# Kernel optimization log

Hardware: AMD Instinct MI355X
Metric: run time of the kernel (lower is better)

## Reference

```python
import jax, jax.numpy as jnp
import numpy as np

N = 8192          # num nodes
F_DIM = 32        # input feature dim
E_DIM = 32        # embedding_dim
SUPPORT = 4       # num relations
NUM_BASES = 2     # basis decomposition size


def setup_inputs() -> dict:
    key = jax.random.key(0)
    k1, k2, k3, k4 = jax.random.split(key, 4)
    features = jax.random.normal(k1, (N, F_DIM), dtype=jnp.float32)
    A = jax.random.normal(k2, (SUPPORT, N, N), dtype=jnp.float32)
    W = jax.random.normal(k3, (NUM_BASES, F_DIM, E_DIM), dtype=jnp.float32) * 0.05
    W_comp = jax.random.normal(k4, (SUPPORT, NUM_BASES), dtype=jnp.float32) * 0.05
    return {"features": features, "A": A, "W": W, "W_comp": W_comp}


def reference(features, A, W, W_comp):
    # Per-relation aggregation: supports[s] = A[s] @ features  -> [S, N, F]
    supports = jnp.einsum('snm,mf->snf', A, features)
    # Concatenate along axis=1 (feature axis): column order is s-major (s*F + f)
    n = features.shape[0]
    supports_ = jnp.transpose(supports, (1, 0, 2)).reshape(n, SUPPORT * F_DIM)
    # Basis decomposition, exactly as original:
    # W: (B, F, E) -> transpose (F, B, E); V = W_comp @ W -> (F, S, E)
    Wt = jnp.transpose(W, (1, 0, 2))                       # [F, B, E]
    V = jnp.einsum('sb,fbe->fse', W_comp, Wt)              # [F, S, E]
    V = V.reshape(SUPPORT * F_DIM, E_DIM)                  # row order f-major (f*S + s), faithful to original
    return supports_ @ V                                   # [N, E]
```

## Files before the change

kernel.cpp:

```cpp
#include <hip/hip_runtime.h>

#define NND 8192
#define FD  32
#define ED  32
#define SUP 4
#define NB  2

#define BROWS 256
#define TK    32
#define CHUNK 2048
#define NSTEP (CHUNK/TK)

#define FMA4(acc, sa, g) { acc.x += (sa) * (g).x; acc.y += (sa) * (g).y; \
                           acc.z += (sa) * (g).z; acc.w += (sa) * (g).w; }

#define GLDS16(gsrc, ldst) \
  __builtin_amdgcn_global_load_lds((const __attribute__((address_space(1))) void*)(gsrc), \
                                   (__attribute__((address_space(3))) void*)(ldst), 16, 0, 0)

__global__ __launch_bounds__(256) void prep_g(
        const float* __restrict__ features,
        const float* __restrict__ W,
        const float* __restrict__ Wc,
        float* __restrict__ G,
        float* __restrict__ out) {
    __shared__ __align__(16) float Vlds[FD * ED];
    const int t   = threadIdx.x;
    const int gid = blockIdx.x * 256 + t;
    const int s   = gid >> 13;
    const int m   = gid & (NND - 1);

    for (int i = t; i < FD * ED; i += 256) {
        const int e  = i & 31;
        const int f  = i >> 5;
        const int f2 = s * 8 + (f >> 2);
        const int s2 = f & 3;
        float v = 0.f;
        #pragma unroll
        for (int b = 0; b < NB; ++b)
            v += Wc[s2 * NB + b] * W[(b * FD + f2) * ED + e];
        Vlds[i] = v;
    }
    __syncthreads();

    float4* out4 = (float4*)out;
    const float4 z = {0.f, 0.f, 0.f, 0.f};
    out4[gid]         = z;
    out4[gid + 32768] = z;

    const float4* feat4 = (const float4*)(features + (size_t)m * FD);
    float4 fr[8];
    #pragma unroll
    for (int i = 0; i < 8; ++i) fr[i] = feat4[i];

    float4 acc[8];
    #pragma unroll
    for (int i = 0; i < 8; ++i) acc[i] = z;

    const float4* V4 = (const float4*)Vlds;
    #pragma unroll
    for (int f = 0; f < FD; ++f) {
        const float fv = ((const float*)fr)[f];
        #pragma unroll
        for (int e4 = 0; e4 < 8; ++e4) {
            const float4 v = V4[f * 8 + e4];
            FMA4(acc[e4], fv, v);
        }
    }
    float4* g4 = (float4*)(G + ((size_t)s * NND + m) * ED);
    #pragma unroll
    for (int e4 = 0; e4 < 8; ++e4) g4[e4] = acc[e4];
}

__global__ __launch_bounds__(128, 1) void rgcn_main(
        const float* __restrict__ A,
        const float* __restrict__ G,
        float* __restrict__ out) {
    __shared__ __align__(16) float Asb[2][BROWS * TK];
    __shared__ __align__(16) float Gsb[2][TK * ED];

    const int t  = threadIdx.x;
    const int bx = blockIdx.x;
    const int nb = bx & 31;
    const int kb = bx >> 5;
    const int s       = kb >> 2;
    const int m_start = (kb & 3) * CHUNK;
    const int n0      = nb * BROWS;

    const float* Ab = A + ((size_t)s * NND + n0) * NND + m_start;
    const float* Gb = G + (size_t)s * NND * ED + (size_t)m_start * ED;

    const int w    = t >> 6;
    const int lane = t & 63;
    const int lr   = lane >> 3;
    const int lc   = lane & 7;

    auto stage = [&](int step, int buf) {
        const int m0 = step * TK;
        #pragma unroll
        for (int i = 0; i < 16; ++i) {
            const int inst = w * 16 + i;
            const int row  = inst * 8 + lr;
            const int c4   = lc ^ (inst & 7);
            GLDS16(Ab + (size_t)row * NND + m0 + (c4 << 2), &Asb[buf][inst * 256]);
        }
        #pragma unroll
        for (int i = 0; i < 2; ++i) {
            const int inst = w * 2 + i;
            GLDS16(Gb + (size_t)m0 * ED + inst * 256 + lane * 4, &Gsb[buf][inst * 256]);
        }
    };

    const int rg = t >> 2;
    const int eg = t & 3;
    const int sw = rg & 7;

    float4 acc[8][2];
    #pragma unroll
    for (int i = 0; i < 8; ++i) {
        acc[i][0] = float4{0.f, 0.f, 0.f, 0.f};
        acc[i][1] = float4{0.f, 0.f, 0.f, 0.f};
    }

    stage(0, 0);
    __syncthreads();

    for (int step = 0; step < NSTEP; ++step) {
        const int buf = step & 1;
        if (step + 1 < NSTEP) stage(step + 1, buf ^ 1);

        const float* As = Asb[buf];
        const float* Gs = Gsb[buf];
        #pragma unroll
        for (int k4 = 0; k4 < 8; ++k4) {
            float4 a[8];
            #pragma unroll
            for (int i = 0; i < 8; ++i)
                a[i] = *(const float4*)&As[(rg * 8 + i) * TK + ((k4 ^ sw) << 2)];
            float4 g[4][2];
            #pragma unroll
            for (int kk = 0; kk < 4; ++kk) {
                g[kk][0] = *(const float4*)&Gs[(k4 * 4 + kk) * ED + eg * 8];
                g[kk][1] = *(const float4*)&Gs[(k4 * 4 + kk) * ED + eg * 8 + 4];
            }
            #pragma unroll
            for (int i = 0; i < 8; ++i) {
                #pragma unroll
                for (int h = 0; h < 2; ++h) {
                    FMA4(acc[i][h], a[i].x, g[0][h]);
                    FMA4(acc[i][h], a[i].y, g[1][h]);
                    FMA4(acc[i][h], a[i].z, g[2][h]);
                    FMA4(acc[i][h], a[i].w, g[3][h]);
                }
            }
        }
        __syncthreads();
    }

    #pragma unroll
    for (int i = 0; i < 8; ++i) {
        float* p = out + (size_t)(n0 + rg * 8 + i) * ED + eg * 8;
        #pragma unroll
        for (int h = 0; h < 2; ++h) {
            atomicAdd(p + h * 4 + 0, acc[i][h].x);
            atomicAdd(p + h * 4 + 1, acc[i][h].y);
            atomicAdd(p + h * 4 + 2, acc[i][h].z);
            atomicAdd(p + h * 4 + 3, acc[i][h].w);
        }
    }
}

extern "C" void kernel_launch(void* const* d_in, const int* in_sizes, int n_in,
                              void* d_out, int out_size, void* d_ws, size_t ws_size,
                              hipStream_t stream) {
    const float* features = (const float*)d_in[0];
    const float* A        = (const float*)d_in[1];
    const float* W        = (const float*)d_in[2];
    const float* Wc       = (const float*)d_in[3];
    float* out = (float*)d_out;
    float* G   = (float*)d_ws;

    prep_g<<<128, 256, 0, stream>>>(features, W, Wc, G, out);
    rgcn_main<<<32 * 16, 128, 0, stream>>>(A, G, out);
}
```

Baseline: 1.551 ms.

## Raise occupancy: 256-thread blocks, TK=16, 8-way K split, strided row mapping

Reworks the main GEMV-like kernel to use 256 threads per block with a halved K tile, an 8-way K split (1024 blocks), and fewer accumulators per thread (4 rows strided by 64 instead of 8 contiguous rows). The LDS swizzle and global-to-LDS staging are rewritten for the 16-wide tile. The aim is more waves resident per CU to better hide memory latency on the bandwidth-bound stream of A. In exchange it doubles the number of output atomics and lowers per-thread register reuse.

```diff
diff --git a/kernel.cpp b/kernel.cpp
--- a/kernel.cpp
+++ b/kernel.cpp
@@ -7,9 +7,10 @@
 #define NB  2
 
 #define BROWS 256
-#define TK    32
-#define CHUNK 2048
-#define NSTEP (CHUNK/TK)
+#define TK    16
+#define KSPLIT 8
+#define CHUNK (NND / KSPLIT)
+#define NSTEP (CHUNK / TK)
 
 #define FMA4(acc, sa, g) { acc.x += (sa) * (g).x; acc.y += (sa) * (g).y; \
                            acc.z += (sa) * (g).z; acc.w += (sa) * (g).w; }
@@ -72,7 +73,7 @@
     for (int e4 = 0; e4 < 8; ++e4) g4[e4] = acc[e4];
 }
 
-__global__ __launch_bounds__(128, 1) void rgcn_main(
+__global__ __launch_bounds__(256, 4) void rgcn_main(
         const float* __restrict__ A,
         const float* __restrict__ G,
         float* __restrict__ out) {
@@ -83,8 +84,8 @@
     const int bx = blockIdx.x;
     const int nb = bx & 31;
     const int kb = bx >> 5;
-    const int s       = kb >> 2;
-    const int m_start = (kb & 3) * CHUNK;
+    const int s       = kb >> 3;
+    const int m_start = (kb & 7) * CHUNK;
     const int n0      = nb * BROWS;
 
     const float* Ab = A + ((size_t)s * NND + n0) * NND + m_start;
@@ -92,32 +93,28 @@
 
     const int w    = t >> 6;
     const int lane = t & 63;
-    const int lr   = lane >> 3;
-    const int lc   = lane & 7;
 
+    const int rowi = lane >> 2;
+    const int sg   = (lane & 3) ^ ((lane >> 3) & 3);
     auto stage = [&](int step, int buf) {
         const int m0 = step * TK;
         #pragma unroll
-        for (int i = 0; i < 16; ++i) {
-            const int inst = w * 16 + i;
-            const int row  = inst * 8 + lr;
-            const int c4   = lc ^ (inst & 7);
-            GLDS16(Ab + (size_t)row * NND + m0 + (c4 << 2), &Asb[buf][inst * 256]);
+        for (int i = 0; i < 4; ++i) {
+            const int inst = w * 4 + i;
+            const int row  = inst * 16 + rowi;
+            GLDS16(Ab + (size_t)row * NND + m0 + (sg << 2), &Asb[buf][inst * 256]);
         }
-        #pragma unroll
-        for (int i = 0; i < 2; ++i) {
-            const int inst = w * 2 + i;
-            GLDS16(Gb + (size_t)m0 * ED + inst * 256 + lane * 4, &Gsb[buf][inst * 256]);
-        }
+        if (w < 2)
+            GLDS16(Gb + (size_t)m0 * ED + w * 256 + lane * 4, &Gsb[buf][w * 256]);
     };
 
     const int rg = t >> 2;
     const int eg = t & 3;
-    const int sw = rg & 7;
+    const int sr = (rg >> 1) & 3;
 
-    float4 acc[8][2];
+    float4 acc[4][2];
     #pragma unroll
-    for (int i = 0; i < 8; ++i) {
+    for (int i = 0; i < 4; ++i) {
         acc[i][0] = float4{0.f, 0.f, 0.f, 0.f};
         acc[i][1] = float4{0.f, 0.f, 0.f, 0.f};
     }
@@ -132,41 +129,35 @@
         const float* As = Asb[buf];
         const float* Gs = Gsb[buf];
         #pragma unroll
-        for (int k4 = 0; k4 < 8; ++k4) {
-            float4 a[8];
-            #pragma unroll
-            for (int i = 0; i < 8; ++i)
-                a[i] = *(const float4*)&As[(rg * 8 + i) * TK + ((k4 ^ sw) << 2)];
-            float4 g[4][2];
-            #pragma unroll
-            for (int kk = 0; kk < 4; ++kk) {
-                g[kk][0] = *(const float4*)&Gs[(k4 * 4 + kk) * ED + eg * 8];
-                g[kk][1] = *(const float4*)&Gs[(k4 * 4 + kk) * ED + eg * 8 + 4];
-            }
-            #pragma unroll
-            for (int i = 0; i < 8; ++i) {
-                #pragma unroll
-                for (int h = 0; h < 2; ++h) {
-                    FMA4(acc[i][h], a[i].x, g[0][h]);
-                    FMA4(acc[i][h], a[i].y, g[1][h]);
-                    FMA4(acc[i][h], a[i].z, g[2][h]);
-                    FMA4(acc[i][h], a[i].w, g[3][h]);
-                }
-            }
+        for (int k4 = 0; k4 < TK / 4; ++k4) {
+            const float4 a0 = *(const float4*)&As[(rg +   0) * TK + ((k4 ^ sr) << 2)];
+            const float4 a1 = *(const float4*)&As[(rg +  64) * TK + ((k4 ^ sr) << 2)];
+            const float4 a2 = *(const float4*)&As[(rg + 128) * TK + ((k4 ^ sr) << 2)];
+            const float4 a3 = *(const float4*)&As[(rg + 192) * TK + ((k4 ^ sr) << 2)];
+            #define KSTEP(kk, comp) { \
+                const float4 g0 = *(const float4*)&Gs[(k4 * 4 + kk) * ED + eg * 8]; \
+                const float4 g1 = *(const float4*)&Gs[(k4 * 4 + kk) * ED + eg * 8 + 4]; \
+                FMA4(acc[0][0], a0.comp, g0); FMA4(acc[0][1], a0.comp, g1); \
+                FMA4(acc[1][0], a1.comp, g0); FMA4(acc[1][1], a1.comp, g1); \
+                FMA4(acc[2][0], a2.comp, g0); FMA4(acc[2][1], a2.comp, g1); \
+                FMA4(acc[3][0], a3.comp, g0); FMA4(acc[3][1], a3.comp, g1); }
+            KSTEP(0, x) KSTEP(1, y) KSTEP(2, z) KSTEP(3, w)
+            #undef KSTEP
         }
         __syncthreads();
     }
 
     #pragma unroll
-    for (int i = 0; i < 8; ++i) {
-        float* p = out + (size_t)(n0 + rg * 8 + i) * ED + eg * 8;
-        #pragma unroll
-        for (int h = 0; h < 2; ++h) {
-            atomicAdd(p + h * 4 + 0, acc[i][h].x);
-            atomicAdd(p + h * 4 + 1, acc[i][h].y);
-            atomicAdd(p + h * 4 + 2, acc[i][h].z);
-            atomicAdd(p + h * 4 + 3, acc[i][h].w);
-        }
+    for (int i = 0; i < 4; ++i) {
+        float* p = out + (size_t)(n0 + rg + 64 * i) * ED + eg * 8;
+        atomicAdd(p + 0, acc[i][0].x);
+        atomicAdd(p + 1, acc[i][0].y);
+        atomicAdd(p + 2, acc[i][0].z);
+        atomicAdd(p + 3, acc[i][0].w);
+        atomicAdd(p + 4, acc[i][1].x);
+        atomicAdd(p + 5, acc[i][1].y);
+        atomicAdd(p + 6, acc[i][1].z);
+        atomicAdd(p + 7, acc[i][1].w);
     }
 }
 
@@ -181,5 +172,5 @@
     float* G   = (float*)d_ws;
 
     prep_g<<<128, 256, 0, stream>>>(features, W, Wc, G, out);
-    rgcn_main<<<32 * 16, 128, 0, stream>>>(A, G, out);
+    rgcn_main<<<32 * KSPLIT * SUP, 256, 0, stream>>>(A, G, out);
 }
```

Result: slower. 1.818 ms (+17.2%).
